# Optimization experiments

Hardware: AMD Instinct MI355X
Metric: run time of the kernel (lower is better)

The kernel has to match this reference:

```python
import jax, jax.numpy as jnp
import numpy as np

N = 10000      # nodes
E = 160000     # directed edges (avg degree 16)
F_IN = 2208    # num_features (DenseNet-161 dim)
H = 512        # hidden_channels
C = 2          # num_classes


def setup_inputs() -> dict:
    key = jax.random.key(0)
    ks = jax.random.split(key, 10)
    x = jax.random.normal(ks[0], (N, F_IN), dtype=jnp.float32)
    edge_index = jax.random.randint(ks[1], (2, E), 0, N, dtype=jnp.int64)
    batch = jnp.zeros((N,), dtype=jnp.int64)

    def glorot(k, fan_in, fan_out):
        s = np.sqrt(6.0 / (fan_in + fan_out)).astype(np.float32)
        return jax.random.uniform(k, (fan_in, fan_out), jnp.float32, -s, s)

    return {
        "x": x,
        "edge_index": edge_index,
        "batch": batch,
        "W1": glorot(ks[2], F_IN, H), "b1": jnp.zeros((H,), jnp.float32),
        "W2": glorot(ks[3], H, H),    "b2": jnp.zeros((H,), jnp.float32),
        "W3": glorot(ks[4], H, H),    "b3": jnp.zeros((H,), jnp.float32),
        "W4": glorot(ks[5], H, C),    "b4": jnp.zeros((C,), jnp.float32),
    }


def reference(x, edge_index, batch, W1, b1, W2, b2, W3, b3, W4, b4):
    # GCNConv (PyG defaults): add self-loops, symmetric normalization
    # out = D^{-1/2} (A + I) D^{-1/2} X W + b. Norm depends only on the
    # graph, so compute it once and reuse across the 4 layers.
    src, dst = edge_index[0], edge_index[1]
    loop = jnp.arange(N, dtype=edge_index.dtype)
    s = jnp.concatenate([src, loop])  # [E+N]
    d = jnp.concatenate([dst, loop])  # [E+N]
    deg = jax.ops.segment_sum(jnp.ones(E + N, x.dtype), d, num_segments=N)
    dinv = jnp.where(deg > 0, jax.lax.rsqrt(deg), 0.0)
    norm = dinv[s] * dinv[d]          # [E+N] per-edge weight

    def conv(h, W, b):
        h = h @ W                                 # [N, out] dense GEMM first (PyG order)
        msg = h[s] * norm[:, None]                # gather + scale  [E+N, out]
        return jax.ops.segment_sum(msg, d, num_segments=N) + b

    h = jax.nn.relu(conv(x, W1, b1))   # dropout p=0.3 is identity in eval mode
    h = jax.nn.relu(conv(h, W2, b2))
    h = jax.nn.relu(conv(h, W3, b3))
    h = conv(h, W4, b4)
    return jax.nn.log_softmax(h, axis=1)
```

## Files before the change

### kernel.cpp

```cpp
#include <hip/hip_runtime.h>
#include <hip/hip_bf16.h>

#define NNODES 10000
#define NEDGES 160000
#define FIN    2208
#define HDIM   512
#define NCLS   2

#define MPAD   10240
#define K1PAD  2240
#define BCAP   128

typedef __bf16 bf16x8 __attribute__((ext_vector_type(8)));
typedef float  f32x4  __attribute__((ext_vector_type(4)));
typedef unsigned short u16x8 __attribute__((ext_vector_type(8)));

__device__ inline unsigned short f2bf(float f) {
    union { float f; unsigned int u; } v; v.f = f;
    return (unsigned short)((v.u + 0x7FFFu + ((v.u >> 16) & 1u)) >> 16);
}
__device__ inline float bf2f(unsigned short u) {
    union { unsigned int i; float f; } v; v.i = ((unsigned int)u) << 16; return v.f;
}

__global__ void k_prep(const float* __restrict__ W1, const float* __restrict__ W2,
                       const float* __restrict__ W3, unsigned short* __restrict__ W1t,
                       unsigned short* __restrict__ W2t, unsigned short* __restrict__ W3t,
                       int* __restrict__ cnt) {
    int n = blockIdx.y;
    int bx = blockIdx.x;
    int t = threadIdx.x;
    if (bx < 9) {
        int k = bx * 256 + t;
        if (k < K1PAD) {
            float v = (k < FIN) ? W1[(size_t)k * HDIM + n] : 0.0f;
            W1t[(size_t)n * K1PAD + k] = f2bf(v);
        }
    } else if (bx < 11) {
        int k = (bx - 9) * 256 + t;
        W2t[(size_t)n * HDIM + k] = f2bf(W2[(size_t)k * HDIM + n]);
    } else if (bx < 13) {
        int k = (bx - 11) * 256 + t;
        W3t[(size_t)n * HDIM + k] = f2bf(W3[(size_t)k * HDIM + n]);
    } else {
        int i = n * 256 + t;
        if (i < NNODES) cnt[i] = 0;
    }
}

__global__ void k_cvt_fill(const float* __restrict__ x, unsigned short* __restrict__ xb,
                           const int* __restrict__ ei, int* __restrict__ cnt,
                           int* __restrict__ bucket) {
    int bx = blockIdx.x;
    int t = threadIdx.x;
    if (bx >= MPAD) {
        int i = (bx - MPAD) * 256 + t;
        if (i < NEDGES) {
            int src = ei[i];
            int dst = ei[NEDGES + i];
            int pos = atomicAdd(&cnt[dst], 1);
            bucket[dst * BCAP + pos] = src;
        }
        return;
    }
    int row = bx;
    unsigned short* orow = xb + (size_t)row * K1PAD;
    u16x8 z = {0, 0, 0, 0, 0, 0, 0, 0};
    if (row >= NNODES) {
        for (int c = t; c < K1PAD / 8; c += 256) *(u16x8*)(orow + c * 8) = z;
        return;
    }
    const float* irow = x + (size_t)row * FIN;
    for (int c = t; c < K1PAD / 8; c += 256) {
        int col = c * 8;
        u16x8 o = z;
        if (col + 8 <= FIN) {
            float4 f0 = *(const float4*)(irow + col);
            float4 f1 = *(const float4*)(irow + col + 4);
            o[0] = f2bf(f0.x); o[1] = f2bf(f0.y); o[2] = f2bf(f0.z); o[3] = f2bf(f0.w);
            o[4] = f2bf(f1.x); o[5] = f2bf(f1.y); o[6] = f2bf(f1.z); o[7] = f2bf(f1.w);
        }
        *(u16x8*)(orow + col) = o;
    }
}

#define BKK 64
#define GG1 640

__device__ __forceinline__ void gemm_body(
    const unsigned short* __restrict__ A, const unsigned short* __restrict__ Bt,
    unsigned short* __restrict__ C, int M, int K, int l) {
    __shared__ char As[128 * BKK * 2] __attribute__((aligned(16)));
    __shared__ char Bs[64 * BKK * 2]  __attribute__((aligned(16)));
    const int tid  = threadIdx.x;
    const int lane = tid & 63;
    const int w    = tid >> 6;
    const int wm   = w & 1, wn = w >> 1;
    const int quad = lane >> 4, lq = lane & 15;

    const int xcd   = l & 7;
    const int q     = l >> 3;
    const int strip = (q >> 3) * 8 + xcd;
    const int bm    = strip * 128;
    const int bn    = (q & 7) * 64;

    f32x4 acc[4][2] = {};

    for (int k0 = 0; k0 < K; k0 += BKK) {
        #pragma unroll
        for (int i = 0; i < 4; ++i) {
            int c = i * 256 + tid;
            int r = c >> 3;
            int g = (c & 7) ^ (r & 7);
            const char* gpA = (const char*)A + ((size_t)(bm + r) * K + k0) * 2 + (g << 4);
            __builtin_amdgcn_global_load_lds(
                (const __attribute__((address_space(1))) void*)gpA,
                (__attribute__((address_space(3))) void*)(As + c * 16), 16, 0, 0);
        }
        #pragma unroll
        for (int i = 0; i < 2; ++i) {
            int c = i * 256 + tid;
            int r = c >> 3;
            int g = (c & 7) ^ (r & 7);
            const char* gpB = (const char*)Bt + ((size_t)(bn + r) * K + k0) * 2 + (g << 4);
            __builtin_amdgcn_global_load_lds(
                (const __attribute__((address_space(1))) void*)gpB,
                (__attribute__((address_space(3))) void*)(Bs + c * 16), 16, 0, 0);
        }
        __syncthreads();

        #pragma unroll
        for (int s = 0; s < 2; ++s) {
            bf16x8 af[4], bfr[2];
            int g = s * 4 + quad;
            #pragma unroll
            for (int i = 0; i < 4; ++i) {
                int r = wm * 64 + i * 16 + lq;
                af[i] = *(const bf16x8*)(As + r * 128 + ((g ^ (r & 7)) << 4));
            }
            #pragma unroll
            for (int j = 0; j < 2; ++j) {
                int n = wn * 32 + j * 16 + lq;
                bfr[j] = *(const bf16x8*)(Bs + n * 128 + ((g ^ (n & 7)) << 4));
            }
            #pragma unroll
            for (int i = 0; i < 4; ++i)
                #pragma unroll
                for (int j = 0; j < 2; ++j)
                    acc[i][j] = __builtin_amdgcn_mfma_f32_16x16x32_bf16(
                        af[i], bfr[j], acc[i][j], 0, 0, 0);
        }
        __syncthreads();
    }

    #pragma unroll
    for (int i = 0; i < 4; ++i) {
        #pragma unroll
        for (int p = 0; p < 4; ++p) {
            int r = bm + wm * 64 + i * 16 + quad * 4 + p;
            if (r < M) {
                #pragma unroll
                for (int j = 0; j < 2; ++j) {
                    int col = bn + wn * 32 + j * 16 + lq;
                    C[(size_t)r * HDIM + col] = f2bf(acc[i][j][p]);
                }
            }
        }
    }
}

__global__ __launch_bounds__(256) void k_gemm1_dinv(
    const unsigned short* __restrict__ A, const unsigned short* __restrict__ Bt,
    unsigned short* __restrict__ C, int M, int K,
    const int* __restrict__ cnt, float* __restrict__ dinv) {
    int bx = blockIdx.x;
    if (bx < GG1) { gemm_body(A, Bt, C, M, K, bx); return; }
    int i = (bx - GG1) * 256 + threadIdx.x;
    if (i < NNODES) dinv[i] = rsqrtf((float)cnt[i] + 1.0f);
}

__global__ __launch_bounds__(256) void k_gemm_bf16(
    const unsigned short* __restrict__ A, const unsigned short* __restrict__ Bt,
    unsigned short* __restrict__ C, int M, int K) {
    gemm_body(A, Bt, C, M, K, blockIdx.x);
}


__global__ void k_agg(const unsigned short* __restrict__ Y, const float* __restrict__ dinv,
                      const int* __restrict__ cnt, const int* __restrict__ bucket,
                      const float* __restrict__ bias, unsigned short* __restrict__ Hb) {
    int w = (blockIdx.x * blockDim.x + threadIdx.x) >> 6;
    int lane = threadIdx.x & 63;
    if (w >= MPAD) return;
    unsigned short* hr = Hb + (size_t)w * HDIM + lane * 8;
    if (w >= NNODES) {
        u16x8 z = {0, 0, 0, 0, 0, 0, 0, 0};
        *(u16x8*)hr = z;
        return;
    }
    float di = dinv[w];
    float sw = di * di;
    u16x8 own = *(const u16x8*)(Y + (size_t)w * HDIM + lane * 8);
    float acc[8];
    #pragma unroll
    for (int t = 0; t < 8; ++t) acc[t] = sw * bf2f(own[t]);

    const int* col = bucket + w * BCAP;
    int deg = cnt[w];
    int e = 0;
    for (; e + 4 <= deg; e += 4) {
        int s0 = col[e + 0], s1 = col[e + 1];
        int s2 = col[e + 2], s3 = col[e + 3];
        float w0 = di * dinv[s0], w1 = di * dinv[s1];
        float w2 = di * dinv[s2], w3 = di * dinv[s3];
        u16x8 v0 = *(const u16x8*)(Y + (size_t)s0 * HDIM + lane * 8);
        u16x8 v1 = *(const u16x8*)(Y + (size_t)s1 * HDIM + lane * 8);
        u16x8 v2 = *(const u16x8*)(Y + (size_t)s2 * HDIM + lane * 8);
        u16x8 v3 = *(const u16x8*)(Y + (size_t)s3 * HDIM + lane * 8);
        #pragma unroll
        for (int t = 0; t < 8; ++t) {
            acc[t] += w0 * bf2f(v0[t]);
            acc[t] += w1 * bf2f(v1[t]);
            acc[t] += w2 * bf2f(v2[t]);
            acc[t] += w3 * bf2f(v3[t]);
        }
    }
    for (; e < deg; ++e) {
        int s = col[e];
        float wg = di * dinv[s];
        u16x8 v = *(const u16x8*)(Y + (size_t)s * HDIM + lane * 8);
        #pragma unroll
        for (int t = 0; t < 8; ++t) acc[t] += wg * bf2f(v[t]);
    }

    float4 b0 = ((const float4*)bias)[lane * 2];
    float4 b1 = ((const float4*)bias)[lane * 2 + 1];
    acc[0] += b0.x; acc[1] += b0.y; acc[2] += b0.z; acc[3] += b0.w;
    acc[4] += b1.x; acc[5] += b1.y; acc[6] += b1.z; acc[7] += b1.w;
    u16x8 o;
    #pragma unroll
    for (int t = 0; t < 8; ++t) o[t] = f2bf(fmaxf(acc[t], 0.0f));
    *(u16x8*)hr = o;
}


__global__ void k_agg_g4(const unsigned short* __restrict__ Y, const float* __restrict__ dinv,
                         const int* __restrict__ cnt, const int* __restrict__ bucket,
                         const float* __restrict__ b3, const float* __restrict__ W4,
                         float* __restrict__ Y4) {
    int w = (blockIdx.x * blockDim.x + threadIdx.x) >> 6;
    int lane = threadIdx.x & 63;
    if (w >= NNODES) return;
    float di = dinv[w];
    float sw = di * di;
    u16x8 own = *(const u16x8*)(Y + (size_t)w * HDIM + lane * 8);
    float acc[8];
    #pragma unroll
    for (int t = 0; t < 8; ++t) acc[t] = sw * bf2f(own[t]);

    const int* col = bucket + w * BCAP;
    int deg = cnt[w];
    int e = 0;
    for (; e + 4 <= deg; e += 4) {
        int s0 = col[e + 0], s1 = col[e + 1];
        int s2 = col[e + 2], s3 = col[e + 3];
        float w0 = di * dinv[s0], w1 = di * dinv[s1];
        float w2 = di * dinv[s2], w3 = di * dinv[s3];
        u16x8 v0 = *(const u16x8*)(Y + (size_t)s0 * HDIM + lane * 8);
        u16x8 v1 = *(const u16x8*)(Y + (size_t)s1 * HDIM + lane * 8);
        u16x8 v2 = *(const u16x8*)(Y + (size_t)s2 * HDIM + lane * 8);
        u16x8 v3 = *(const u16x8*)(Y + (size_t)s3 * HDIM + lane * 8);
        #pragma unroll
        for (int t = 0; t < 8; ++t) {
            acc[t] += w0 * bf2f(v0[t]);
            acc[t] += w1 * bf2f(v1[t]);
            acc[t] += w2 * bf2f(v2[t]);
            acc[t] += w3 * bf2f(v3[t]);
        }
    }
    for (; e < deg; ++e) {
        int s = col[e];
        float wg = di * dinv[s];
        u16x8 v = *(const u16x8*)(Y + (size_t)s * HDIM + lane * 8);
        #pragma unroll
        for (int t = 0; t < 8; ++t) acc[t] += wg * bf2f(v[t]);
    }

    float4 b0 = ((const float4*)b3)[lane * 2];
    float4 b1 = ((const float4*)b3)[lane * 2 + 1];
    acc[0] += b0.x; acc[1] += b0.y; acc[2] += b0.z; acc[3] += b0.w;
    acc[4] += b1.x; acc[5] += b1.y; acc[6] += b1.z; acc[7] += b1.w;
    #pragma unroll
    for (int t = 0; t < 8; ++t) acc[t] = fmaxf(acc[t], 0.0f);

    const float4* wf = (const float4*)W4;
    float4 w0 = wf[lane * 4 + 0];
    float4 w1 = wf[lane * 4 + 1];
    float4 w2 = wf[lane * 4 + 2];
    float4 w3 = wf[lane * 4 + 3];
    float z0 = acc[0]*w0.x + acc[1]*w0.z + acc[2]*w1.x + acc[3]*w1.z
             + acc[4]*w2.x + acc[5]*w2.z + acc[6]*w3.x + acc[7]*w3.z;
    float z1 = acc[0]*w0.y + acc[1]*w0.w + acc[2]*w1.y + acc[3]*w1.w
             + acc[4]*w2.y + acc[5]*w2.w + acc[6]*w3.y + acc[7]*w3.w;
    #pragma unroll
    for (int off = 32; off > 0; off >>= 1) {
        z0 += __shfl_down(z0, off);
        z1 += __shfl_down(z1, off);
    }
    if (lane == 0) {
        Y4[2 * w] = z0;
        Y4[2 * w + 1] = z1;
    }
}


__global__ void k_final(const float* __restrict__ Y4, const float* __restrict__ dinv,
                        const int* __restrict__ cnt, const int* __restrict__ bucket,
                        const float* __restrict__ b4, float* __restrict__ out, int n) {
    int i = blockIdx.x * blockDim.x + threadIdx.x;
    if (i >= n) return;
    float di = dinv[i];
    float sw = di * di;
    float z0 = sw * Y4[2 * i];
    float z1 = sw * Y4[2 * i + 1];
    const int* col = bucket + i * BCAP;
    int deg = cnt[i];
    for (int e = 0; e < deg; ++e) {
        int s = col[e];
        float wgt = di * dinv[s];
        z0 += wgt * Y4[2 * s];
        z1 += wgt * Y4[2 * s + 1];
    }
    z0 += b4[0];
    z1 += b4[1];
    float m = fmaxf(z0, z1);
    float l = m + logf(expf(z0 - m) + expf(z1 - m));
    out[2 * i] = z0 - l;
    out[2 * i + 1] = z1 - l;
}


extern "C" void kernel_launch(void* const* d_in, const int* in_sizes, int n_in,
                              void* d_out, int out_size, void* d_ws, size_t ws_size,
                              hipStream_t stream) {
    const float* x  = (const float*)d_in[0];
    const int*   ei = (const int*)d_in[1];
    const float* W1 = (const float*)d_in[3];
    const float* b1 = (const float*)d_in[4];
    const float* W2 = (const float*)d_in[5];
    const float* b2 = (const float*)d_in[6];
    const float* W3 = (const float*)d_in[7];
    const float* b3 = (const float*)d_in[8];
    const float* W4 = (const float*)d_in[9];
    const float* b4 = (const float*)d_in[10];
    float* out = (float*)d_out;

    char* ws = (char*)d_ws;
    float*          dinv    = (float*)(ws + 0);
    int*            cnt     = (int*)  (ws + 40960);
    int*            bucket  = (int*)  (ws + 81920);
    float*          Y4      = (float*)(ws + 5201920);
    unsigned short* xb      = (unsigned short*)(ws + 5283840);
    unsigned short* W1t     = (unsigned short*)(ws + 51159040);
    unsigned short* W2t     = (unsigned short*)(ws + 53452800);
    unsigned short* W3t     = (unsigned short*)(ws + 53977088);
    unsigned short* Yb      = (unsigned short*)(ws + 54501376);
    unsigned short* Hb      = (unsigned short*)(ws + 64987136);
    if (ws_size < 75472896) return;

    const int agrid = (MPAD * 64) / 256;

    k_prep<<<dim3(14, HDIM), 256, 0, stream>>>(W1, W2, W3, W1t, W2t, W3t, cnt);
    k_cvt_fill<<<MPAD + 625, 256, 0, stream>>>(x, xb, ei, cnt, bucket);
    k_gemm1_dinv<<<GG1 + 40, 256, 0, stream>>>(xb, W1t, Yb, NNODES, K1PAD, cnt, dinv);
    k_agg<<<agrid, 256, 0, stream>>>(Yb, dinv, cnt, bucket, b1, Hb);
    k_gemm_bf16<<<GG1, 256, 0, stream>>>(Hb, W2t, Yb, NNODES, HDIM);
    k_agg<<<agrid, 256, 0, stream>>>(Yb, dinv, cnt, bucket, b2, Hb);
    k_gemm_bf16<<<GG1, 256, 0, stream>>>(Hb, W3t, Yb, NNODES, HDIM);
    k_agg_g4<<<(NNODES * 64) / 256, 256, 0, stream>>>(Yb, dinv, cnt, bucket, b3, W4, Y4);
    k_final<<<40, 256, 0, stream>>>(Y4, dinv, cnt, bucket, b4, out, NNODES);
}
```

Measured before the change: 310.5 us.

## Split aggregation into column chunks per block to improve gather cache locality

The aggregation kernels now give each wave one 128-column slice of a node row instead of the full 512 columns. Block indices are swizzled so that blocks handling the same column chunk for nearby node groups run together, which aims to keep the gathered slice of Y resident in L2. The edge loop is unrolled to 8 gathers for more memory-level parallelism. The final fused layer-4 projection now combines partial dot products with atomics, so Y4 is zeroed in the prep kernel; in exchange, neighbor indices and dinv are read four times and each gather moves only 4 bytes per lane.

```diff
diff --git a/kernel.cpp b/kernel.cpp
--- a/kernel.cpp
+++ b/kernel.cpp
@@ -26,7 +26,7 @@
 __global__ void k_prep(const float* __restrict__ W1, const float* __restrict__ W2,
                        const float* __restrict__ W3, unsigned short* __restrict__ W1t,
                        unsigned short* __restrict__ W2t, unsigned short* __restrict__ W3t,
-                       int* __restrict__ cnt) {
+                       int* __restrict__ cnt, float* __restrict__ Y4) {
     int n = blockIdx.y;
     int bx = blockIdx.x;
     int t = threadIdx.x;
@@ -45,6 +45,7 @@
     } else {
         int i = n * 256 + t;
         if (i < NNODES) cnt[i] = 0;
+        if (i < 2 * MPAD) Y4[i] = 0.0f;
     }
 }
 
@@ -185,131 +186,81 @@
     gemm_body(A, Bt, C, M, K, blockIdx.x);
 }
 
-
-__global__ void k_agg(const unsigned short* __restrict__ Y, const float* __restrict__ dinv,
-                      const int* __restrict__ cnt, const int* __restrict__ bucket,
-                      const float* __restrict__ bias, unsigned short* __restrict__ Hb) {
-    int w = (blockIdx.x * blockDim.x + threadIdx.x) >> 6;
+template<int FUSE4>
+__global__ void k_agg_c(const unsigned short* __restrict__ Y, const float* __restrict__ dinv,
+                        const int* __restrict__ cnt, const int* __restrict__ bucket,
+                        const float* __restrict__ bias, unsigned short* __restrict__ Hb,
+                        const float* __restrict__ W4, float* __restrict__ Y4) {
+    int b = blockIdx.x;
     int lane = threadIdx.x & 63;
-    if (w >= MPAD) return;
-    unsigned short* hr = Hb + (size_t)w * HDIM + lane * 8;
+    int wid = threadIdx.x >> 6;
+    int c = (b & 7) >> 1;
+    int group = ((b >> 3) << 1) | (b & 1);
+    int w = group * 4 + wid;
+    int col = c * 128 + lane * 2;
     if (w >= NNODES) {
-        u16x8 z = {0, 0, 0, 0, 0, 0, 0, 0};
-        *(u16x8*)hr = z;
+        if (!FUSE4) *(unsigned int*)(Hb + (size_t)w * HDIM + col) = 0;
         return;
     }
     float di = dinv[w];
     float sw = di * di;
-    u16x8 own = *(const u16x8*)(Y + (size_t)w * HDIM + lane * 8);
-    float acc[8];
-    #pragma unroll
-    for (int t = 0; t < 8; ++t) acc[t] = sw * bf2f(own[t]);
-
-    const int* col = bucket + w * BCAP;
+    const unsigned short* yc = Y + col;
+    unsigned int ov = *(const unsigned int*)(yc + (size_t)w * HDIM);
+    float a0 = sw * bf2f((unsigned short)ov);
+    float a1 = sw * bf2f((unsigned short)(ov >> 16));
+
+    const int* colp = bucket + w * BCAP;
     int deg = cnt[w];
     int e = 0;
-    for (; e + 4 <= deg; e += 4) {
-        int s0 = col[e + 0], s1 = col[e + 1];
-        int s2 = col[e + 2], s3 = col[e + 3];
-        float w0 = di * dinv[s0], w1 = di * dinv[s1];
-        float w2 = di * dinv[s2], w3 = di * dinv[s3];
-        u16x8 v0 = *(const u16x8*)(Y + (size_t)s0 * HDIM + lane * 8);
-        u16x8 v1 = *(const u16x8*)(Y + (size_t)s1 * HDIM + lane * 8);
-        u16x8 v2 = *(const u16x8*)(Y + (size_t)s2 * HDIM + lane * 8);
-        u16x8 v3 = *(const u16x8*)(Y + (size_t)s3 * HDIM + lane * 8);
-        #pragma unroll
-        for (int t = 0; t < 8; ++t) {
-            acc[t] += w0 * bf2f(v0[t]);
-            acc[t] += w1 * bf2f(v1[t]);
-            acc[t] += w2 * bf2f(v2[t]);
-            acc[t] += w3 * bf2f(v3[t]);
-        }
+    for (; e + 8 <= deg; e += 8) {
+        int s0 = colp[e + 0], s1 = colp[e + 1], s2 = colp[e + 2], s3 = colp[e + 3];
+        int s4 = colp[e + 4], s5 = colp[e + 5], s6 = colp[e + 6], s7 = colp[e + 7];
+        float w0 = di * dinv[s0], w1 = di * dinv[s1], w2 = di * dinv[s2], w3 = di * dinv[s3];
+        float w4 = di * dinv[s4], w5 = di * dinv[s5], w6 = di * dinv[s6], w7 = di * dinv[s7];
+        unsigned int v0 = *(const unsigned int*)(yc + (size_t)s0 * HDIM);
+        unsigned int v1 = *(const unsigned int*)(yc + (size_t)s1 * HDIM);
+        unsigned int v2 = *(const unsigned int*)(yc + (size_t)s2 * HDIM);
+        unsigned int v3 = *(const unsigned int*)(yc + (size_t)s3 * HDIM);
+        unsigned int v4 = *(const unsigned int*)(yc + (size_t)s4 * HDIM);
+        unsigned int v5 = *(const unsigned int*)(yc + (size_t)s5 * HDIM);
+        unsigned int v6 = *(const unsigned int*)(yc + (size_t)s6 * HDIM);
+        unsigned int v7 = *(const unsigned int*)(yc + (size_t)s7 * HDIM);
+        a0 += w0 * bf2f((unsigned short)v0); a1 += w0 * bf2f((unsigned short)(v0 >> 16));
+        a0 += w1 * bf2f((unsigned short)v1); a1 += w1 * bf2f((unsigned short)(v1 >> 16));
+        a0 += w2 * bf2f((unsigned short)v2); a1 += w2 * bf2f((unsigned short)(v2 >> 16));
+        a0 += w3 * bf2f((unsigned short)v3); a1 += w3 * bf2f((unsigned short)(v3 >> 16));
+        a0 += w4 * bf2f((unsigned short)v4); a1 += w4 * bf2f((unsigned short)(v4 >> 16));
+        a0 += w5 * bf2f((unsigned short)v5); a1 += w5 * bf2f((unsigned short)(v5 >> 16));
+        a0 += w6 * bf2f((unsigned short)v6); a1 += w6 * bf2f((unsigned short)(v6 >> 16));
+        a0 += w7 * bf2f((unsigned short)v7); a1 += w7 * bf2f((unsigned short)(v7 >> 16));
     }
     for (; e < deg; ++e) {
-        int s = col[e];
+        int s = colp[e];
         float wg = di * dinv[s];
-        u16x8 v = *(const u16x8*)(Y + (size_t)s * HDIM + lane * 8);
-        #pragma unroll
-        for (int t = 0; t < 8; ++t) acc[t] += wg * bf2f(v[t]);
-    }
-
-    float4 b0 = ((const float4*)bias)[lane * 2];
-    float4 b1 = ((const float4*)bias)[lane * 2 + 1];
-    acc[0] += b0.x; acc[1] += b0.y; acc[2] += b0.z; acc[3] += b0.w;
-    acc[4] += b1.x; acc[5] += b1.y; acc[6] += b1.z; acc[7] += b1.w;
-    u16x8 o;
-    #pragma unroll
-    for (int t = 0; t < 8; ++t) o[t] = f2bf(fmaxf(acc[t], 0.0f));
-    *(u16x8*)hr = o;
-}
-
-
-__global__ void k_agg_g4(const unsigned short* __restrict__ Y, const float* __restrict__ dinv,
-                         const int* __restrict__ cnt, const int* __restrict__ bucket,
-                         const float* __restrict__ b3, const float* __restrict__ W4,
-                         float* __restrict__ Y4) {
-    int w = (blockIdx.x * blockDim.x + threadIdx.x) >> 6;
-    int lane = threadIdx.x & 63;
-    if (w >= NNODES) return;
-    float di = dinv[w];
-    float sw = di * di;
-    u16x8 own = *(const u16x8*)(Y + (size_t)w * HDIM + lane * 8);
-    float acc[8];
-    #pragma unroll
-    for (int t = 0; t < 8; ++t) acc[t] = sw * bf2f(own[t]);
-
-    const int* col = bucket + w * BCAP;
-    int deg = cnt[w];
-    int e = 0;
-    for (; e + 4 <= deg; e += 4) {
-        int s0 = col[e + 0], s1 = col[e + 1];
-        int s2 = col[e + 2], s3 = col[e + 3];
-        float w0 = di * dinv[s0], w1 = di * dinv[s1];
-        float w2 = di * dinv[s2], w3 = di * dinv[s3];
-        u16x8 v0 = *(const u16x8*)(Y + (size_t)s0 * HDIM + lane * 8);
-        u16x8 v1 = *(const u16x8*)(Y + (size_t)s1 * HDIM + lane * 8);
-        u16x8 v2 = *(const u16x8*)(Y + (size_t)s2 * HDIM + lane * 8);
-        u16x8 v3 = *(const u16x8*)(Y + (size_t)s3 * HDIM + lane * 8);
-        #pragma unroll
-        for (int t = 0; t < 8; ++t) {
-            acc[t] += w0 * bf2f(v0[t]);
-            acc[t] += w1 * bf2f(v1[t]);
-            acc[t] += w2 * bf2f(v2[t]);
-            acc[t] += w3 * bf2f(v3[t]);
-        }
-    }
-    for (; e < deg; ++e) {
-        int s = col[e];
-        float wg = di * dinv[s];
-        u16x8 v = *(const u16x8*)(Y + (size_t)s * HDIM + lane * 8);
-        #pragma unroll
-        for (int t = 0; t < 8; ++t) acc[t] += wg * bf2f(v[t]);
-    }
-
-    float4 b0 = ((const float4*)b3)[lane * 2];
-    float4 b1 = ((const float4*)b3)[lane * 2 + 1];
-    acc[0] += b0.x; acc[1] += b0.y; acc[2] += b0.z; acc[3] += b0.w;
-    acc[4] += b1.x; acc[5] += b1.y; acc[6] += b1.z; acc[7] += b1.w;
-    #pragma unroll
-    for (int t = 0; t < 8; ++t) acc[t] = fmaxf(acc[t], 0.0f);
-
-    const float4* wf = (const float4*)W4;
-    float4 w0 = wf[lane * 4 + 0];
-    float4 w1 = wf[lane * 4 + 1];
-    float4 w2 = wf[lane * 4 + 2];
-    float4 w3 = wf[lane * 4 + 3];
-    float z0 = acc[0]*w0.x + acc[1]*w0.z + acc[2]*w1.x + acc[3]*w1.z
-             + acc[4]*w2.x + acc[5]*w2.z + acc[6]*w3.x + acc[7]*w3.z;
-    float z1 = acc[0]*w0.y + acc[1]*w0.w + acc[2]*w1.y + acc[3]*w1.w
-             + acc[4]*w2.y + acc[5]*w2.w + acc[6]*w3.y + acc[7]*w3.w;
-    #pragma unroll
-    for (int off = 32; off > 0; off >>= 1) {
-        z0 += __shfl_down(z0, off);
-        z1 += __shfl_down(z1, off);
-    }
-    if (lane == 0) {
-        Y4[2 * w] = z0;
-        Y4[2 * w + 1] = z1;
+        unsigned int v = *(const unsigned int*)(yc + (size_t)s * HDIM);
+        a0 += wg * bf2f((unsigned short)v);
+        a1 += wg * bf2f((unsigned short)(v >> 16));
+    }
+
+    float2 bb = *(const float2*)(bias + col);
+    a0 = fmaxf(a0 + bb.x, 0.0f);
+    a1 = fmaxf(a1 + bb.y, 0.0f);
+    if (!FUSE4) {
+        unsigned int o = (unsigned int)f2bf(a0) | ((unsigned int)f2bf(a1) << 16);
+        *(unsigned int*)(Hb + (size_t)w * HDIM + col) = o;
+    } else {
+        float4 wv = *(const float4*)(W4 + col * 2);
+        float z0 = a0 * wv.x + a1 * wv.z;
+        float z1 = a0 * wv.y + a1 * wv.w;
+        #pragma unroll
+        for (int off = 32; off > 0; off >>= 1) {
+            z0 += __shfl_down(z0, off);
+            z1 += __shfl_down(z1, off);
+        }
+        if (lane == 0) {
+            atomicAdd(&Y4[2 * w], z0);
+            atomicAdd(&Y4[2 * w + 1], z1);
+        }
     }
 }
 
@@ -368,15 +319,13 @@
     unsigned short* Hb      = (unsigned short*)(ws + 64987136);
     if (ws_size < 75472896) return;
 
-    const int agrid = (MPAD * 64) / 256;
-
-    k_prep<<<dim3(14, HDIM), 256, 0, stream>>>(W1, W2, W3, W1t, W2t, W3t, cnt);
+    k_prep<<<dim3(14, HDIM), 256, 0, stream>>>(W1, W2, W3, W1t, W2t, W3t, cnt, Y4);
     k_cvt_fill<<<MPAD + 625, 256, 0, stream>>>(x, xb, ei, cnt, bucket);
     k_gemm1_dinv<<<GG1 + 40, 256, 0, stream>>>(xb, W1t, Yb, NNODES, K1PAD, cnt, dinv);
-    k_agg<<<agrid, 256, 0, stream>>>(Yb, dinv, cnt, bucket, b1, Hb);
+    k_agg_c<0><<<MPAD, 256, 0, stream>>>(Yb, dinv, cnt, bucket, b1, Hb, nullptr, nullptr);
     k_gemm_bf16<<<GG1, 256, 0, stream>>>(Hb, W2t, Yb, NNODES, HDIM);
-    k_agg<<<agrid, 256, 0, stream>>>(Yb, dinv, cnt, bucket, b2, Hb);
+    k_agg_c<0><<<MPAD, 256, 0, stream>>>(Yb, dinv, cnt, bucket, b2, Hb, nullptr, nullptr);
     k_gemm_bf16<<<GG1, 256, 0, stream>>>(Hb, W3t, Yb, NNODES, HDIM);
-    k_agg_g4<<<(NNODES * 64) / 256, 256, 0, stream>>>(Yb, dinv, cnt, bucket, b3, W4, Y4);
+    k_agg_c<1><<<MPAD, 256, 0, stream>>>(Yb, dinv, cnt, bucket, b3, nullptr, W4, Y4);
     k_final<<<40, 256, 0, stream>>>(Y4, dinv, cnt, bucket, b4, out, NNODES);
 }
```

New measurement: 326.6 us. 5.2% more time.

## Double-buffer GEMM LDS tiles and unroll aggregation gather to eight edges

Applied to the files above, without the earlier changes.

The GEMM now keeps two LDS buffers and prefetches the tile two steps ahead through global_load_lds. It waits with explicit vmcnt counts so the global loads overlap the MFMA work instead of stalling at each k-step. The sparse aggregation loop gathers eight neighbour rows per iteration instead of four, giving more loads in flight. The cost is double the LDS use per block, which may lower occupancy, plus more registers in the gather loop. The hand-set vmcnt(6) must match the six loads issued per stage.

```diff
diff --git a/kernel.cpp b/kernel.cpp
--- a/kernel.cpp
+++ b/kernel.cpp
@@ -90,8 +90,8 @@
 __device__ __forceinline__ void gemm_body(
     const unsigned short* __restrict__ A, const unsigned short* __restrict__ Bt,
     unsigned short* __restrict__ C, int M, int K, int l) {
-    __shared__ char As[128 * BKK * 2] __attribute__((aligned(16)));
-    __shared__ char Bs[64 * BKK * 2]  __attribute__((aligned(16)));
+    __shared__ char As[2][128 * BKK * 2] __attribute__((aligned(16)));
+    __shared__ char Bs[2][64 * BKK * 2]  __attribute__((aligned(16)));
     const int tid  = threadIdx.x;
     const int lane = tid & 63;
     const int w    = tid >> 6;
@@ -105,8 +105,9 @@
     const int bn    = (q & 7) * 64;
 
     f32x4 acc[4][2] = {};
-
-    for (int k0 = 0; k0 < K; k0 += BKK) {
+    const int nk = K / BKK;
+
+    auto stage = [&](int buf, int k0) {
         #pragma unroll
         for (int i = 0; i < 4; ++i) {
             int c = i * 256 + tid;
@@ -115,7 +116,7 @@
             const char* gpA = (const char*)A + ((size_t)(bm + r) * K + k0) * 2 + (g << 4);
             __builtin_amdgcn_global_load_lds(
                 (const __attribute__((address_space(1))) void*)gpA,
-                (__attribute__((address_space(3))) void*)(As + c * 16), 16, 0, 0);
+                (__attribute__((address_space(3))) void*)(As[buf] + c * 16), 16, 0, 0);
         }
         #pragma unroll
         for (int i = 0; i < 2; ++i) {
@@ -125,9 +126,21 @@
             const char* gpB = (const char*)Bt + ((size_t)(bn + r) * K + k0) * 2 + (g << 4);
             __builtin_amdgcn_global_load_lds(
                 (const __attribute__((address_space(1))) void*)gpB,
-                (__attribute__((address_space(3))) void*)(Bs + c * 16), 16, 0, 0);
-        }
-        __syncthreads();
+                (__attribute__((address_space(3))) void*)(Bs[buf] + c * 16), 16, 0, 0);
+        }
+    };
+
+    stage(0, 0);
+    stage(1, BKK);
+    int cur = 0;
+
+    for (int t = 0; t < nk; ++t) {
+        if (t + 1 < nk) {
+            asm volatile("s_waitcnt vmcnt(6)" ::: "memory");
+        } else {
+            asm volatile("s_waitcnt vmcnt(0)" ::: "memory");
+        }
+        __builtin_amdgcn_s_barrier();
 
         #pragma unroll
         for (int s = 0; s < 2; ++s) {
@@ -136,12 +149,12 @@
             #pragma unroll
             for (int i = 0; i < 4; ++i) {
                 int r = wm * 64 + i * 16 + lq;
-                af[i] = *(const bf16x8*)(As + r * 128 + ((g ^ (r & 7)) << 4));
+                af[i] = *(const bf16x8*)(As[cur] + r * 128 + ((g ^ (r & 7)) << 4));
             }
             #pragma unroll
             for (int j = 0; j < 2; ++j) {
                 int n = wn * 32 + j * 16 + lq;
-                bfr[j] = *(const bf16x8*)(Bs + n * 128 + ((g ^ (n & 7)) << 4));
+                bfr[j] = *(const bf16x8*)(Bs[cur] + n * 128 + ((g ^ (n & 7)) << 4));
             }
             #pragma unroll
             for (int i = 0; i < 4; ++i)
@@ -150,7 +163,10 @@
                     acc[i][j] = __builtin_amdgcn_mfma_f32_16x16x32_bf16(
                         af[i], bfr[j], acc[i][j], 0, 0, 0);
         }
-        __syncthreads();
+
+        __builtin_amdgcn_s_barrier();
+        if (t + 2 < nk) stage(cur, (t + 2) * BKK);
+        cur ^= 1;
     }
 
     #pragma unroll
@@ -208,21 +224,29 @@
     const int* col = bucket + w * BCAP;
     int deg = cnt[w];
     int e = 0;
-    for (; e + 4 <= deg; e += 4) {
-        int s0 = col[e + 0], s1 = col[e + 1];
-        int s2 = col[e + 2], s3 = col[e + 3];
-        float w0 = di * dinv[s0], w1 = di * dinv[s1];
-        float w2 = di * dinv[s2], w3 = di * dinv[s3];
+    for (; e + 8 <= deg; e += 8) {
+        int s0 = col[e + 0], s1 = col[e + 1], s2 = col[e + 2], s3 = col[e + 3];
+        int s4 = col[e + 4], s5 = col[e + 5], s6 = col[e + 6], s7 = col[e + 7];
+        float w0 = di * dinv[s0], w1 = di * dinv[s1], w2 = di * dinv[s2], w3 = di * dinv[s3];
+        float w4 = di * dinv[s4], w5 = di * dinv[s5], w6 = di * dinv[s6], w7 = di * dinv[s7];
         u16x8 v0 = *(const u16x8*)(Y + (size_t)s0 * HDIM + lane * 8);
         u16x8 v1 = *(const u16x8*)(Y + (size_t)s1 * HDIM + lane * 8);
         u16x8 v2 = *(const u16x8*)(Y + (size_t)s2 * HDIM + lane * 8);
         u16x8 v3 = *(const u16x8*)(Y + (size_t)s3 * HDIM + lane * 8);
+        u16x8 v4 = *(const u16x8*)(Y + (size_t)s4 * HDIM + lane * 8);
+        u16x8 v5 = *(const u16x8*)(Y + (size_t)s5 * HDIM + lane * 8);
+        u16x8 v6 = *(const u16x8*)(Y + (size_t)s6 * HDIM + lane * 8);
+        u16x8 v7 = *(const u16x8*)(Y + (size_t)s7 * HDIM + lane * 8);
         #pragma unroll
         for (int t = 0; t < 8; ++t) {
             acc[t] += w0 * bf2f(v0[t]);
             acc[t] += w1 * bf2f(v1[t]);
             acc[t] += w2 * bf2f(v2[t]);
             acc[t] += w3 * bf2f(v3[t]);
+            acc[t] += w4 * bf2f(v4[t]);
+            acc[t] += w5 * bf2f(v5[t]);
+            acc[t] += w6 * bf2f(v6[t]);
+            acc[t] += w7 * bf2f(v7[t]);
         }
     }
     for (; e < deg; ++e) {
```

Result: slower. 319.3 us (+2.8%).

## Fuse whole GCN forward into one cooperative persistent kernel with grid syncs

Applied to the files above, without the earlier changes.

Replaces the nine-kernel launch sequence with a single cooperative kernel of 640 blocks that runs weight prep, x conversion, edge bucketing, three GEMMs, the aggregations and the final log-softmax, separated by grid-wide barriers. The dinv array is dropped and the normalisation is recomputed inline from the degree counts, and the aggregation loop is unrolled eight edges at a time. The aim is to remove kernel launch gaps and tail effects. In exchange every phase is limited to 640 blocks, the extra rsqrt per edge adds work, and the old multi-kernel path stays only as a fallback if the cooperative launch fails.

```diff
diff --git a/kernel.cpp b/kernel.cpp
--- a/kernel.cpp
+++ b/kernel.cpp
@@ -1,5 +1,8 @@
 #include <hip/hip_runtime.h>
 #include <hip/hip_bf16.h>
+#include <hip/hip_cooperative_groups.h>
+
+namespace cg = cooperative_groups;
 
 #define NNODES 10000
 #define NEDGES 160000
@@ -10,6 +13,7 @@
 #define MPAD   10240
 #define K1PAD  2240
 #define BCAP   128
+#define GRID   640
 
 typedef __bf16 bf16x8 __attribute__((ext_vector_type(8)));
 typedef float  f32x4  __attribute__((ext_vector_type(4)));
@@ -21,67 +25,6 @@
 }
 __device__ inline float bf2f(unsigned short u) {
     union { unsigned int i; float f; } v; v.i = ((unsigned int)u) << 16; return v.f;
-}
-
-__global__ void k_prep(const float* __restrict__ W1, const float* __restrict__ W2,
-                       const float* __restrict__ W3, unsigned short* __restrict__ W1t,
-                       unsigned short* __restrict__ W2t, unsigned short* __restrict__ W3t,
-                       int* __restrict__ cnt) {
-    int n = blockIdx.y;
-    int bx = blockIdx.x;
-    int t = threadIdx.x;
-    if (bx < 9) {
-        int k = bx * 256 + t;
-        if (k < K1PAD) {
-            float v = (k < FIN) ? W1[(size_t)k * HDIM + n] : 0.0f;
-            W1t[(size_t)n * K1PAD + k] = f2bf(v);
-        }
-    } else if (bx < 11) {
-        int k = (bx - 9) * 256 + t;
-        W2t[(size_t)n * HDIM + k] = f2bf(W2[(size_t)k * HDIM + n]);
-    } else if (bx < 13) {
-        int k = (bx - 11) * 256 + t;
-        W3t[(size_t)n * HDIM + k] = f2bf(W3[(size_t)k * HDIM + n]);
-    } else {
-        int i = n * 256 + t;
-        if (i < NNODES) cnt[i] = 0;
-    }
-}
-
-__global__ void k_cvt_fill(const float* __restrict__ x, unsigned short* __restrict__ xb,
-                           const int* __restrict__ ei, int* __restrict__ cnt,
-                           int* __restrict__ bucket) {
-    int bx = blockIdx.x;
-    int t = threadIdx.x;
-    if (bx >= MPAD) {
-        int i = (bx - MPAD) * 256 + t;
-        if (i < NEDGES) {
-            int src = ei[i];
-            int dst = ei[NEDGES + i];
-            int pos = atomicAdd(&cnt[dst], 1);
-            bucket[dst * BCAP + pos] = src;
-        }
-        return;
-    }
-    int row = bx;
-    unsigned short* orow = xb + (size_t)row * K1PAD;
-    u16x8 z = {0, 0, 0, 0, 0, 0, 0, 0};
-    if (row >= NNODES) {
-        for (int c = t; c < K1PAD / 8; c += 256) *(u16x8*)(orow + c * 8) = z;
-        return;
-    }
-    const float* irow = x + (size_t)row * FIN;
-    for (int c = t; c < K1PAD / 8; c += 256) {
-        int col = c * 8;
-        u16x8 o = z;
-        if (col + 8 <= FIN) {
-            float4 f0 = *(const float4*)(irow + col);
-            float4 f1 = *(const float4*)(irow + col + 4);
-            o[0] = f2bf(f0.x); o[1] = f2bf(f0.y); o[2] = f2bf(f0.z); o[3] = f2bf(f0.w);
-            o[4] = f2bf(f1.x); o[5] = f2bf(f1.y); o[6] = f2bf(f1.z); o[7] = f2bf(f1.w);
-        }
-        *(u16x8*)(orow + col) = o;
-    }
 }
 
 #define BKK 64
@@ -169,6 +112,272 @@
     }
 }
 
+template<int FUSE4>
+__device__ __forceinline__ void agg_node(
+    const unsigned short* __restrict__ Y, const int* __restrict__ cnt,
+    const int* __restrict__ bucket, const float* __restrict__ bias,
+    unsigned short* __restrict__ Hb, const float* __restrict__ W4,
+    float* __restrict__ Y4, int w, int lane)
+{
+    if (!FUSE4 && w >= NNODES) {
+        u16x8 z = {0, 0, 0, 0, 0, 0, 0, 0};
+        *(u16x8*)(Hb + (size_t)w * HDIM + lane * 8) = z;
+        return;
+    }
+    float di = rsqrtf((float)cnt[w] + 1.0f);
+    float sw = di * di;
+    u16x8 own = *(const u16x8*)(Y + (size_t)w * HDIM + lane * 8);
+    float acc[8];
+    #pragma unroll
+    for (int t = 0; t < 8; ++t) acc[t] = sw * bf2f(own[t]);
+
+    const int* col = bucket + w * BCAP;
+    int deg = cnt[w];
+    int e = 0;
+    for (; e + 8 <= deg; e += 8) {
+        int s0 = col[e + 0], s1 = col[e + 1], s2 = col[e + 2], s3 = col[e + 3];
+        int s4 = col[e + 4], s5 = col[e + 5], s6 = col[e + 6], s7 = col[e + 7];
+        float w0 = di * rsqrtf((float)cnt[s0] + 1.0f);
+        float w1 = di * rsqrtf((float)cnt[s1] + 1.0f);
+        float w2 = di * rsqrtf((float)cnt[s2] + 1.0f);
+        float w3 = di * rsqrtf((float)cnt[s3] + 1.0f);
+        float w4 = di * rsqrtf((float)cnt[s4] + 1.0f);
+        float w5 = di * rsqrtf((float)cnt[s5] + 1.0f);
+        float w6 = di * rsqrtf((float)cnt[s6] + 1.0f);
+        float w7 = di * rsqrtf((float)cnt[s7] + 1.0f);
+        u16x8 v0 = *(const u16x8*)(Y + (size_t)s0 * HDIM + lane * 8);
+        u16x8 v1 = *(const u16x8*)(Y + (size_t)s1 * HDIM + lane * 8);
+        u16x8 v2 = *(const u16x8*)(Y + (size_t)s2 * HDIM + lane * 8);
+        u16x8 v3 = *(const u16x8*)(Y + (size_t)s3 * HDIM + lane * 8);
+        u16x8 v4 = *(const u16x8*)(Y + (size_t)s4 * HDIM + lane * 8);
+        u16x8 v5 = *(const u16x8*)(Y + (size_t)s5 * HDIM + lane * 8);
+        u16x8 v6 = *(const u16x8*)(Y + (size_t)s6 * HDIM + lane * 8);
+        u16x8 v7 = *(const u16x8*)(Y + (size_t)s7 * HDIM + lane * 8);
+        #pragma unroll
+        for (int t = 0; t < 8; ++t) {
+            acc[t] += w0 * bf2f(v0[t]);
+            acc[t] += w1 * bf2f(v1[t]);
+            acc[t] += w2 * bf2f(v2[t]);
+            acc[t] += w3 * bf2f(v3[t]);
+            acc[t] += w4 * bf2f(v4[t]);
+            acc[t] += w5 * bf2f(v5[t]);
+            acc[t] += w6 * bf2f(v6[t]);
+            acc[t] += w7 * bf2f(v7[t]);
+        }
+    }
+    for (; e < deg; ++e) {
+        int s = col[e];
+        float wg = di * rsqrtf((float)cnt[s] + 1.0f);
+        u16x8 v = *(const u16x8*)(Y + (size_t)s * HDIM + lane * 8);
+        #pragma unroll
+        for (int t = 0; t < 8; ++t) acc[t] += wg * bf2f(v[t]);
+    }
+
+    float4 b0 = ((const float4*)bias)[lane * 2];
+    float4 b1 = ((const float4*)bias)[lane * 2 + 1];
+    acc[0] += b0.x; acc[1] += b0.y; acc[2] += b0.z; acc[3] += b0.w;
+    acc[4] += b1.x; acc[5] += b1.y; acc[6] += b1.z; acc[7] += b1.w;
+
+    if (!FUSE4) {
+        u16x8 o;
+        #pragma unroll
+        for (int t = 0; t < 8; ++t) o[t] = f2bf(fmaxf(acc[t], 0.0f));
+        *(u16x8*)(Hb + (size_t)w * HDIM + lane * 8) = o;
+    } else {
+        #pragma unroll
+        for (int t = 0; t < 8; ++t) acc[t] = fmaxf(acc[t], 0.0f);
+        const float4* wf = (const float4*)W4;
+        float4 w0 = wf[lane * 4 + 0];
+        float4 w1 = wf[lane * 4 + 1];
+        float4 w2 = wf[lane * 4 + 2];
+        float4 w3 = wf[lane * 4 + 3];
+        float z0 = acc[0]*w0.x + acc[1]*w0.z + acc[2]*w1.x + acc[3]*w1.z
+                 + acc[4]*w2.x + acc[5]*w2.z + acc[6]*w3.x + acc[7]*w3.z;
+        float z1 = acc[0]*w0.y + acc[1]*w0.w + acc[2]*w1.y + acc[3]*w1.w
+                 + acc[4]*w2.y + acc[5]*w2.w + acc[6]*w3.y + acc[7]*w3.w;
+        #pragma unroll
+        for (int off = 32; off > 0; off >>= 1) {
+            z0 += __shfl_down(z0, off);
+            z1 += __shfl_down(z1, off);
+        }
+        if (lane == 0) {
+            Y4[2 * w] = z0;
+            Y4[2 * w + 1] = z1;
+        }
+    }
+}
+
+__global__ __launch_bounds__(256, 3) void k_fused(
+    const float* __restrict__ x, const int* __restrict__ ei,
+    const float* __restrict__ W1, const float* __restrict__ b1,
+    const float* __restrict__ W2, const float* __restrict__ b2,
+    const float* __restrict__ W3, const float* __restrict__ b3,
+    const float* __restrict__ W4, const float* __restrict__ b4,
+    float* __restrict__ out,
+    int* __restrict__ cnt, int* __restrict__ bucket, float* __restrict__ Y4,
+    unsigned short* __restrict__ xb, unsigned short* __restrict__ W1t,
+    unsigned short* __restrict__ W2t, unsigned short* __restrict__ W3t,
+    unsigned short* __restrict__ Yb, unsigned short* __restrict__ Hb)
+{
+    cg::grid_group grid = cg::this_grid();
+    const int tid  = threadIdx.x;
+    const int bid  = blockIdx.x;
+    const int lane = tid & 63;
+    const int gwave = bid * 4 + (tid >> 6);
+
+    for (int u = bid; u < 14 * HDIM; u += GRID) {
+        int bx = u % 14;
+        int n  = u / 14;
+        if (bx < 9) {
+            int k = bx * 256 + tid;
+            if (k < K1PAD) {
+                float v = (k < FIN) ? W1[(size_t)k * HDIM + n] : 0.0f;
+                W1t[(size_t)n * K1PAD + k] = f2bf(v);
+            }
+        } else if (bx < 11) {
+            int k = (bx - 9) * 256 + tid;
+            W2t[(size_t)n * HDIM + k] = f2bf(W2[(size_t)k * HDIM + n]);
+        } else if (bx < 13) {
+            int k = (bx - 11) * 256 + tid;
+            W3t[(size_t)n * HDIM + k] = f2bf(W3[(size_t)k * HDIM + n]);
+        } else {
+            int i = n * 256 + tid;
+            if (i < NNODES) cnt[i] = 0;
+        }
+    }
+    for (int row = bid; row < MPAD; row += GRID) {
+        unsigned short* orow = xb + (size_t)row * K1PAD;
+        u16x8 z = {0, 0, 0, 0, 0, 0, 0, 0};
+        if (row >= NNODES) {
+            for (int c = tid; c < K1PAD / 8; c += 256) *(u16x8*)(orow + c * 8) = z;
+        } else {
+            const float* irow = x + (size_t)row * FIN;
+            for (int c = tid; c < K1PAD / 8; c += 256) {
+                int col = c * 8;
+                u16x8 o = z;
+                if (col + 8 <= FIN) {
+                    float4 f0 = *(const float4*)(irow + col);
+                    float4 f1 = *(const float4*)(irow + col + 4);
+                    o[0] = f2bf(f0.x); o[1] = f2bf(f0.y); o[2] = f2bf(f0.z); o[3] = f2bf(f0.w);
+                    o[4] = f2bf(f1.x); o[5] = f2bf(f1.y); o[6] = f2bf(f1.z); o[7] = f2bf(f1.w);
+                }
+                *(u16x8*)(orow + col) = o;
+            }
+        }
+    }
+    grid.sync();
+
+    for (int i = bid * 256 + tid; i < NEDGES; i += GRID * 256) {
+        int src = ei[i];
+        int dst = ei[NEDGES + i];
+        int pos = atomicAdd(&cnt[dst], 1);
+        bucket[dst * BCAP + pos] = src;
+    }
+    gemm_body(xb, W1t, Yb, NNODES, K1PAD, bid);
+    grid.sync();
+
+    for (int w = gwave; w < MPAD; w += 2560)
+        agg_node<0>(Yb, cnt, bucket, b1, Hb, nullptr, nullptr, w, lane);
+    grid.sync();
+
+    gemm_body(Hb, W2t, Yb, NNODES, HDIM, bid);
+    grid.sync();
+
+    for (int w = gwave; w < MPAD; w += 2560)
+        agg_node<0>(Yb, cnt, bucket, b2, Hb, nullptr, nullptr, w, lane);
+    grid.sync();
+
+    gemm_body(Hb, W3t, Yb, NNODES, HDIM, bid);
+    grid.sync();
+
+    for (int w = gwave; w < NNODES; w += 2560)
+        agg_node<1>(Yb, cnt, bucket, b3, nullptr, W4, Y4, w, lane);
+    grid.sync();
+
+    for (int i = bid * 256 + tid; i < NNODES; i += GRID * 256) {
+        float di = rsqrtf((float)cnt[i] + 1.0f);
+        float sw = di * di;
+        float z0 = sw * Y4[2 * i];
+        float z1 = sw * Y4[2 * i + 1];
+        const int* col = bucket + i * BCAP;
+        int deg = cnt[i];
+        for (int e = 0; e < deg; ++e) {
+            int s = col[e];
+            float wgt = di * rsqrtf((float)cnt[s] + 1.0f);
+            z0 += wgt * Y4[2 * s];
+            z1 += wgt * Y4[2 * s + 1];
+        }
+        z0 += b4[0];
+        z1 += b4[1];
+        float m = fmaxf(z0, z1);
+        float l = m + logf(expf(z0 - m) + expf(z1 - m));
+        out[2 * i] = z0 - l;
+        out[2 * i + 1] = z1 - l;
+    }
+}
+
+
+__global__ void k_prep(const float* __restrict__ W1, const float* __restrict__ W2,
+                       const float* __restrict__ W3, unsigned short* __restrict__ W1t,
+                       unsigned short* __restrict__ W2t, unsigned short* __restrict__ W3t,
+                       int* __restrict__ cnt) {
+    int n = blockIdx.y;
+    int bx = blockIdx.x;
+    int t = threadIdx.x;
+    if (bx < 9) {
+        int k = bx * 256 + t;
+        if (k < K1PAD) {
+            float v = (k < FIN) ? W1[(size_t)k * HDIM + n] : 0.0f;
+            W1t[(size_t)n * K1PAD + k] = f2bf(v);
+        }
+    } else if (bx < 11) {
+        int k = (bx - 9) * 256 + t;
+        W2t[(size_t)n * HDIM + k] = f2bf(W2[(size_t)k * HDIM + n]);
+    } else if (bx < 13) {
+        int k = (bx - 11) * 256 + t;
+        W3t[(size_t)n * HDIM + k] = f2bf(W3[(size_t)k * HDIM + n]);
+    } else {
+        int i = n * 256 + t;
+        if (i < NNODES) cnt[i] = 0;
+    }
+}
+
+__global__ void k_cvt_fill(const float* __restrict__ x, unsigned short* __restrict__ xb,
+                           const int* __restrict__ ei, int* __restrict__ cnt,
+                           int* __restrict__ bucket) {
+    int bx = blockIdx.x;
+    int t = threadIdx.x;
+    if (bx >= MPAD) {
+        int i = (bx - MPAD) * 256 + t;
+        if (i < NEDGES) {
+            int src = ei[i];
+            int dst = ei[NEDGES + i];
+            int pos = atomicAdd(&cnt[dst], 1);
+            bucket[dst * BCAP + pos] = src;
+        }
+        return;
+    }
+    int row = bx;
+    unsigned short* orow = xb + (size_t)row * K1PAD;
+    u16x8 z = {0, 0, 0, 0, 0, 0, 0, 0};
+    if (row >= NNODES) {
+        for (int c = t; c < K1PAD / 8; c += 256) *(u16x8*)(orow + c * 8) = z;
+        return;
+    }
+    const float* irow = x + (size_t)row * FIN;
+    for (int c = t; c < K1PAD / 8; c += 256) {
+        int col = c * 8;
+        u16x8 o = z;
+        if (col + 8 <= FIN) {
+            float4 f0 = *(const float4*)(irow + col);
+            float4 f1 = *(const float4*)(irow + col + 4);
+            o[0] = f2bf(f0.x); o[1] = f2bf(f0.y); o[2] = f2bf(f0.z); o[3] = f2bf(f0.w);
+            o[4] = f2bf(f1.x); o[5] = f2bf(f1.y); o[6] = f2bf(f1.z); o[7] = f2bf(f1.w);
+        }
+        *(u16x8*)(orow + col) = o;
+    }
+}
+
 __global__ __launch_bounds__(256) void k_gemm1_dinv(
     const unsigned short* __restrict__ A, const unsigned short* __restrict__ Bt,
     unsigned short* __restrict__ C, int M, int K,
@@ -184,7 +393,6 @@
     unsigned short* __restrict__ C, int M, int K) {
     gemm_body(A, Bt, C, M, K, blockIdx.x);
 }
-
 
 __global__ void k_agg(const unsigned short* __restrict__ Y, const float* __restrict__ dinv,
                       const int* __restrict__ cnt, const int* __restrict__ bucket,
@@ -243,7 +451,6 @@
     *(u16x8*)hr = o;
 }
 
-
 __global__ void k_agg_g4(const unsigned short* __restrict__ Y, const float* __restrict__ dinv,
                          const int* __restrict__ cnt, const int* __restrict__ bucket,
                          const float* __restrict__ b3, const float* __restrict__ W4,
@@ -312,7 +519,6 @@
         Y4[2 * w + 1] = z1;
     }
 }
-
 
 __global__ void k_final(const float* __restrict__ Y4, const float* __restrict__ dinv,
                         const int* __restrict__ cnt, const int* __restrict__ bucket,
@@ -368,8 +574,19 @@
     unsigned short* Hb      = (unsigned short*)(ws + 64987136);
     if (ws_size < 75472896) return;
 
+    void* args[] = { (void*)&x, (void*)&ei,
+                     (void*)&W1, (void*)&b1, (void*)&W2, (void*)&b2,
+                     (void*)&W3, (void*)&b3, (void*)&W4, (void*)&b4,
+                     (void*)&out,
+                     (void*)&cnt, (void*)&bucket, (void*)&Y4,
+                     (void*)&xb, (void*)&W1t, (void*)&W2t, (void*)&W3t,
+                     (void*)&Yb, (void*)&Hb };
+    hipError_t err = hipLaunchCooperativeKernel((const void*)k_fused,
+        dim3(GRID), dim3(256), args, 0, stream);
+    if (err == hipSuccess) return;
+    (void)hipGetLastError();
+
     const int agrid = (MPAD * 64) / 256;
-
     k_prep<<<dim3(14, HDIM), 256, 0, stream>>>(W1, W2, W3, W1t, W2t, W3t, cnt);
     k_cvt_fill<<<MPAD + 625, 256, 0, stream>>>(x, xb, ei, cnt, bucket);
     k_gemm1_dinv<<<GG1 + 40, 256, 0, stream>>>(xb, W1t, Yb, NNODES, K1PAD, cnt, dinv);
```

Measured after the change: 872.8 us. 2.81x slower.
